# Kernel tuning notes

Measured on AMD Instinct MI355X. Metric: run time of the kernel, lower is better.

The kernel has to match this reference:

```python
import jax, jax.numpy as jnp
import numpy as np

D, DEPTH, HEADS, P, IMG = 768, 12, 12, 16, 224
GRID = IMG // P
NTOK = GRID * GRID + 1  # 197
PLEN, NTASK, NCLS = 5, 5, 100
DEEP = (2, 3, 4)
HD = D // HEADS
LN_EPS = 1e-6


def _ln(x, w, b):
    m = x.mean(-1, keepdims=True)
    v = ((x - m) ** 2).mean(-1, keepdims=True)
    return (x - m) * jax.lax.rsqrt(v + LN_EPS) * w + b


def _l2n(x):
    return x * jax.lax.rsqrt(jnp.maximum((x * x).sum(-1, keepdims=True), 1e-12))


def _mlp(x, w1, b1, w2, b2):
    return jax.nn.gelu(x @ w1.T + b1, approximate=False) @ w2.T + b2


def _mha(x, wqkv, bqkv, wp, bp):
    B, N, _ = x.shape
    qkv = (x @ wqkv.T + bqkv).reshape(B, N, 3, HEADS, HD)
    q, k, v = qkv[:, :, 0], qkv[:, :, 1], qkv[:, :, 2]
    a = jax.nn.softmax(jnp.einsum('bnhd,bmhd->bhnm', q * HD ** -0.5, k), -1)
    o = jnp.einsum('bhnm,bmhd->bnhd', a, v).reshape(B, N, D)
    return o @ wp.T + bp


def _block(x, i, p):
    x = x + _mha(_ln(x, p['ln1_w'][i], p['ln1_b'][i]), p['qkv_w'][i], p['qkv_b'][i], p['proj_w'][i], p['proj_b'][i])
    return x + _mlp(_ln(x, p['ln2_w'][i], p['ln2_b'][i]), p['fc1_w'][i], p['fc1_b'][i], p['fc2_w'][i], p['fc2_b'][i])


def _blocks(x, p):
    for i in range(DEPTH):
        x = _block(x, i, p)
    return x


def _deep_block(x, i, li, prompts, p):
    # single-head prefix-prompt attention exactly as written in the torch module,
    # including the (buggy but faithful) transpose(1,2).reshape(B,N,C) scramble
    B, N, _ = x.shape
    nx = _ln(x, p['ln1_w'][i], p['ln1_b'][i])
    qkv = (nx @ p['qkv_w'][i].T + p['qkv_b'][i]).reshape(B, N, 3, D)
    q, k, v = qkv[:, :, 0], qkv[:, :, 1], qkv[:, :, 2]
    k = jnp.concatenate([prompts[:, 2 * li], k], axis=1)
    v = jnp.concatenate([prompts[:, 2 * li + 1], v], axis=1)
    a = jax.nn.softmax(jnp.einsum('bnd,bmd->bnm', q, k) * HD ** -0.5, -1)
    av = jnp.einsum('bnm,bmd->bnd', a, v)
    av = av.swapaxes(1, 2).reshape(B, N, D)
    x = x + (av @ p['proj_w'][i].T + p['proj_b'][i])
    return x + _mlp(_ln(x, p['ln2_w'][i], p['ln2_b'][i]), p['fc1_w'][i], p['fc1_b'][i], p['fc2_w'][i], p['fc2_b'][i])


def _embed(inputs, patch_w, patch_b, cls_token, pos_embed):
    B = inputs.shape[0]
    x = inputs.reshape(B, 3, GRID, P, GRID, P).transpose(0, 2, 4, 1, 3, 5).reshape(B, GRID * GRID, 3 * P * P)
    x = x @ patch_w.T + patch_b
    x = jnp.concatenate([jnp.broadcast_to(cls_token, (B, 1, D)), x], axis=1)
    return x + pos_embed


def _branch_forward(x, sel_main, main_idx, sub_idx, p, main_prompts, sub_prompt, pos_embed, fc_w, fc_b, norm_w, norm_b):
    B = x.shape[0]
    # ---- main branch: per-sample gathered deep prompts ----
    mx = x[main_idx]
    mp = main_prompts[sel_main].reshape(mx.shape[0], 2 * len(DEEP), PLEN, D)
    for i in range(DEPTH):
        if i in DEEP:
            mx = _deep_block(mx, i, DEEP.index(i), mp, p)
        else:
            mx = _block(mx, i, p)
    mx = _ln(mx, norm_w, norm_b)
    mlog = mx[:, 0] @ fc_w.T + fc_b  # fc_norm is Identity in timm vit_base
    # ---- sub branch: prepend sub prompts after cls ----
    sx = x[sub_idx]
    sp = jnp.broadcast_to(sub_prompt[0] + pos_embed[0, 0], (sx.shape[0], PLEN, D))
    sx = jnp.concatenate([sx[:, :1], sp, sx[:, 1:]], axis=1)
    sx = _ln(_blocks(sx, p), norm_w, norm_b)
    slog = sx[:, 1:1 + PLEN].mean(axis=1) @ fc_w.T + fc_b
    # scatter back to per-sample logits (fixed output shape)
    return jnp.zeros((B, NCLS), x.dtype).at[main_idx].set(mlog).at[sub_idx].set(slog)


def setup_inputs() -> dict:
    key = jax.random.key(0)
    ks = iter(jax.random.split(key, 32))
    nk = lambda: next(ks)
    r = lambda shape, sc=0.02: jax.random.normal(nk(), shape, jnp.float32) * sc
    return {
        'inputs': jax.random.normal(nk(), (16, 3, IMG, IMG), jnp.float32),
        'task_id': 4,
        'patch_w': r((D, 3 * P * P)),
        'patch_b': jnp.zeros((D,)),
        'cls_token': r((1, 1, D)),
        'pos_embed': r((1, NTOK, D)),
        'qkv_w': r((DEPTH, 3 * D, D)),
        'qkv_b': jnp.zeros((DEPTH, 3 * D)),
        'proj_w': r((DEPTH, D, D)),
        'proj_b': jnp.zeros((DEPTH, D)),
        'ln1_w': jnp.ones((DEPTH, D)), 'ln1_b': jnp.zeros((DEPTH, D)),
        'ln2_w': jnp.ones((DEPTH, D)), 'ln2_b': jnp.zeros((DEPTH, D)),
        'fc1_w': r((DEPTH, 4 * D, D)),
        'fc1_b': jnp.zeros((DEPTH, 4 * D)),
        'fc2_w': r((DEPTH, D, 4 * D)),
        'fc2_b': jnp.zeros((DEPTH, D)),
        'norm_w': jnp.ones((D,)), 'norm_b': jnp.zeros((D,)),
        'fc_w': r((NCLS, D)),
        'fc_b': jnp.zeros((NCLS,)),
        'main_key': r((NTASK, D), 1.0),
        'sub_key': r((1, D), 1.0),
        'main_prompts': r((NTASK, 1, 2, len(DEEP), PLEN, D), 1.0),
        'sub_prompt': r((1, PLEN, D), 1.0),
    }


def reference(inputs, task_id, patch_w, patch_b, cls_token, pos_embed, qkv_w, qkv_b, proj_w, proj_b,
              ln1_w, ln1_b, ln2_w, ln2_b, fc1_w, fc1_b, fc2_w, fc2_b, norm_w, norm_b, fc_w, fc_b,
              main_key, sub_key, main_prompts, sub_prompt):
    p = dict(qkv_w=qkv_w, qkv_b=qkv_b, proj_w=proj_w, proj_b=proj_b, ln1_w=ln1_w, ln1_b=ln1_b,
             ln2_w=ln2_w, ln2_b=ln2_b, fc1_w=fc1_w, fc1_b=fc1_b, fc2_w=fc2_w, fc2_b=fc2_b)
    x = _embed(inputs, patch_w, patch_b, cls_token, pos_embed)
    # frozen query pass (torch.no_grad in the original)
    query = _ln(_blocks(x, p), norm_w, norm_b)[:, 0]
    # test-time routing: cosine similarity to [main_key[:task_id+1], sub_key]
    cand = jnp.concatenate([main_key[:task_id + 1], sub_key], axis=0)
    sim = _l2n(query) @ _l2n(cand).T
    sel = jnp.argmax(sim, axis=1)  # selection_size == 1
    main_mask = sel <= task_id
    main_idx = jnp.nonzero(main_mask)[0]
    sub_idx = jnp.nonzero(jnp.logical_not(main_mask))[0]
    sel_main = sel[main_idx]
    return _branch_forward(x, sel_main, main_idx, sub_idx, p, main_prompts, sub_prompt, pos_embed,
                           fc_w, fc_b, norm_w, norm_b)
```

## Files before the change

### kernel.cpp

```cpp
#include <hip/hip_runtime.h>
#include <math.h>

#define B_    16
#define NT_   197
#define NS_   202
#define HEADS_ 12
#define DEPTH_ 12
#define NCLS_ 100
#define MROW_ (B_ * NT_)
#define SROW_ (B_ * NS_)
#define CROW_ (MROW_ + SROW_)

typedef __attribute__((ext_vector_type(8))) short short8v;
typedef __attribute__((ext_vector_type(4))) float f32x4;

__device__ __forceinline__ short f2bf(float f){
    unsigned u = __builtin_bit_cast(unsigned, f);
    unsigned r = (u + 0x7FFFu + ((u >> 16) & 1u)) >> 16;
    return (short)r;
}
__device__ __forceinline__ unsigned pk2(float a, float b){
    return (unsigned)(unsigned short)f2bf(a) | (((unsigned)(unsigned short)f2bf(b)) << 16);
}

__device__ __forceinline__ float block_reduce_sum_f(float s, float* red, int lane, int wid){
#pragma unroll
    for (int off = 32; off; off >>= 1) s += __shfl_xor(s, off);
    if (lane == 0) red[wid] = s;
    __syncthreads();
    float S = red[0] + red[1] + red[2] + red[3];
    __syncthreads();
    return S;
}
__device__ __forceinline__ double block_reduce_sum_d(double s, double* red, int lane, int wid){
#pragma unroll
    for (int off = 32; off; off >>= 1) s += __shfl_xor(s, off);
    if (lane == 0) red[wid] = s;
    __syncthreads();
    double S = red[0] + red[1] + red[2] + red[3];
    __syncthreads();
    return S;
}

__global__ void convert_w_k(const float* __restrict__ in, short* __restrict__ out, long n){
    long i = ((long)blockIdx.x * 256 + threadIdx.x) * 8;
    long stride = (long)gridDim.x * 256 * 8;
    for (; i < n; i += stride){
        float4 a = *(const float4*)(in + i);
        float4 b = *(const float4*)(in + i + 4);
        uint4 o4;
        o4.x = pk2(a.x, a.y); o4.y = pk2(a.z, a.w);
        o4.z = pk2(b.x, b.y); o4.w = pk2(b.z, b.w);
        *(uint4*)(out + i) = o4;
    }
}

template<int EPI, int WB>
__global__ __launch_bounds__(256) void gemm_bf16(
    const short* __restrict__ A, const void* __restrict__ Wv,
    const float* __restrict__ bias, const float* __restrict__ Res,
    float* __restrict__ Cf, short* __restrict__ Cb, int M, int K, int N)
{
    __shared__ short As[128 * 48];
    __shared__ short Bs[128 * 48];
    const int t = threadIdx.x;
    const int lane = t & 63, wid = t >> 6;
    const int wr = wid >> 1, wc = wid & 1;
    const long row0 = (long)blockIdx.y * 128;
    const long col0 = (long)blockIdx.x * 128;

    f32x4 acc[4][4];
#pragma unroll
    for (int i = 0; i < 4; i++)
#pragma unroll
        for (int j = 0; j < 4; j++) acc[i][j] = (f32x4){0.f, 0.f, 0.f, 0.f};

    const int l15 = lane & 15, lkg = lane >> 4;
    const int ar = t >> 2, ac = t & 3;
    const int bn = t >> 1, bh = t & 1;

    for (int k0 = 0; k0 < K; k0 += 32){
#pragma unroll
        for (int it = 0; it < 2; it++){
            int r = ar + it * 64;
            long gr = row0 + r;
            uint4 v = {0u, 0u, 0u, 0u};
            if (gr < M) v = *(const uint4*)(A + gr * K + k0 + ac * 8);
            *(uint4*)(&As[r * 48 + ac * 8]) = v;
        }
        if (WB == 1){
            const short* Wb = (const short*)Wv;
            const short* Wp = Wb + (col0 + bn) * K + k0 + bh * 16;
            uint4 lo = *(const uint4*)(Wp);
            uint4 hi = *(const uint4*)(Wp + 8);
            *(uint4*)(&Bs[bn * 48 + bh * 16])     = lo;
            *(uint4*)(&Bs[bn * 48 + bh * 16 + 8]) = hi;
        } else {
            const float* Wf = (const float*)Wv;
            const float* Wp = Wf + (col0 + bn) * K + k0 + bh * 16;
            unsigned rr[8];
#pragma unroll
            for (int g = 0; g < 8; g++){
                float2 f = *(const float2*)(Wp + g * 2);
                rr[g] = pk2(f.x, f.y);
            }
            uint4 lo = {rr[0], rr[1], rr[2], rr[3]};
            uint4 hi = {rr[4], rr[5], rr[6], rr[7]};
            *(uint4*)(&Bs[bn * 48 + bh * 16])     = lo;
            *(uint4*)(&Bs[bn * 48 + bh * 16 + 8]) = hi;
        }
        __syncthreads();

        short8v a[4], b[4];
#pragma unroll
        for (int i = 0; i < 4; i++)
            a[i] = *(const short8v*)(&As[(wr * 64 + i * 16 + l15) * 48 + lkg * 8]);
#pragma unroll
        for (int j = 0; j < 4; j++)
            b[j] = *(const short8v*)(&Bs[(wc * 64 + j * 16 + l15) * 48 + lkg * 8]);
#pragma unroll
        for (int i = 0; i < 4; i++)
#pragma unroll
            for (int j = 0; j < 4; j++)
                acc[i][j] = __builtin_amdgcn_mfma_f32_16x16x32_bf16(a[i], b[j], acc[i][j], 0, 0, 0);
        __syncthreads();
    }

#pragma unroll
    for (int i = 0; i < 4; i++){
#pragma unroll
        for (int q = 0; q < 4; q++){
            long gr = row0 + wr * 64 + i * 16 + lkg * 4 + q;
            if (gr >= M) continue;
#pragma unroll
            for (int j = 0; j < 4; j++){
                long gc = col0 + wc * 64 + j * 16 + l15;
                float v = acc[i][j][q] + bias[gc];
                if (EPI == 1){
                    v = 0.5f * v * (1.f + erff(v * 0.70710678118654752f));
                    Cb[gr * N + gc] = f2bf(v);
                } else if (EPI == 2){
                    Cf[gr * N + gc] = v + Res[gr * N + gc];
                } else {
                    Cf[gr * N + gc] = v;
                }
            }
        }
    }
}

__global__ __launch_bounds__(256) void ln_k(const float* __restrict__ x,
    const float* __restrict__ w, const float* __restrict__ b,
    short* __restrict__ y)
{
    __shared__ float red[4];
    int row = blockIdx.x, t = threadIdx.x;
    int lane = t & 63, wid = t >> 6;
    const float* xr = x + (long)row * 768;
    float v0 = xr[t], v1 = xr[t + 256], v2 = xr[t + 512];
    float S = block_reduce_sum_f(v0 + v1 + v2, red, lane, wid);
    float m = S * (1.f / 768.f);
    float d0 = v0 - m, d1 = v1 - m, d2 = v2 - m;
    float Q = block_reduce_sum_f(d0*d0 + d1*d1 + d2*d2, red, lane, wid);
    float rs = 1.f / sqrtf(Q * (1.f / 768.f) + 1e-6f);
    short* yr = y + (long)row * 768;
    yr[t]       = f2bf(d0 * rs * w[t]       + b[t]);
    yr[t + 256] = f2bf(d1 * rs * w[t + 256] + b[t + 256]);
    yr[t + 512] = f2bf(d2 * rs * w[t + 512] + b[t + 512]);
}

__global__ __launch_bounds__(512) void attn_mfma(
    const float* __restrict__ qkv0, short* __restrict__ o0, int N0,
    const float* __restrict__ qkv1, short* __restrict__ o1, int N1)
{
    __shared__ short Ks[208 * 72];
    __shared__ short Vs[64 * 232];
    __shared__ short Ps[8 * 16 * 232];
    const int bh = blockIdx.x;
    const int b = bh / HEADS_, h = bh % HEADS_;
    const int seg = blockIdx.y;
    const float* qkv = seg ? qkv1 : qkv0;
    short* o = seg ? o1 : o0;
    const int Ntok = seg ? N1 : N0;
    const int t = threadIdx.x, lane = t & 63, wid = t >> 6;
    const long rb = (long)b * Ntok;

    {
        const int r = t >> 2, c = (t & 3) * 16;
#pragma unroll
        for (int pass = 0; pass < 2; pass++){
            int m = r + pass * 128;
            if (m < 208){
                if (m < Ntok){
                    const float* kr = qkv + (rb + m) * 2304 + 768  + h * 64 + c;
                    const float* vr = qkv + (rb + m) * 2304 + 1536 + h * 64 + c;
#pragma unroll
                    for (int j = 0; j < 16; j += 4){
                        float4 f = *(const float4*)(kr + j);
                        *(unsigned*)(&Ks[m * 72 + c + j])     = pk2(f.x, f.y);
                        *(unsigned*)(&Ks[m * 72 + c + j + 2]) = pk2(f.z, f.w);
                    }
#pragma unroll
                    for (int j = 0; j < 16; j += 4){
                        float4 f = *(const float4*)(vr + j);
                        Vs[(c + j    ) * 232 + m] = f2bf(f.x);
                        Vs[(c + j + 1) * 232 + m] = f2bf(f.y);
                        Vs[(c + j + 2) * 232 + m] = f2bf(f.z);
                        Vs[(c + j + 3) * 232 + m] = f2bf(f.w);
                    }
                } else {
#pragma unroll
                    for (int j = 0; j < 16; j += 2)
                        *(unsigned*)(&Ks[m * 72 + c + j]) = 0u;
#pragma unroll
                    for (int j = 0; j < 16; j++)
                        Vs[(c + j) * 232 + m] = 0;
                }
            }
        }
        for (int i = t; i < 64 * 16; i += 512){
            int d = i >> 4, m = 208 + (i & 15);
            Vs[d * 232 + m] = 0;
        }
        for (int i = t; i < 8 * 16 * 16; i += 512){
            int w = i >> 8, rr = (i >> 4) & 15, m = 208 + (i & 15);
            Ps[(w * 16 + rr) * 232 + m] = 0;
        }
    }
    __syncthreads();

    const int l15 = lane & 15, lkg = lane >> 4;
    short* Pw = &Ps[wid * 16 * 232];

    for (int s = wid; s < 13; s += 8){
        const int q0 = s * 16;
        short8v a0, a1;
        {
            int qrow = q0 + l15;
            if (qrow < Ntok){
                const float* qp = qkv + (rb + qrow) * 2304 + h * 64;
                float4 f0 = *(const float4*)(qp + lkg * 8);
                float4 f1 = *(const float4*)(qp + lkg * 8 + 4);
                float4 f2 = *(const float4*)(qp + 32 + lkg * 8);
                float4 f3 = *(const float4*)(qp + 32 + lkg * 8 + 4);
                unsigned u0 = pk2(f0.x * 0.125f, f0.y * 0.125f);
                unsigned u1 = pk2(f0.z * 0.125f, f0.w * 0.125f);
                unsigned u2 = pk2(f1.x * 0.125f, f1.y * 0.125f);
                unsigned u3 = pk2(f1.z * 0.125f, f1.w * 0.125f);
                unsigned v0 = pk2(f2.x * 0.125f, f2.y * 0.125f);
                unsigned v1 = pk2(f2.z * 0.125f, f2.w * 0.125f);
                unsigned v2 = pk2(f3.x * 0.125f, f3.y * 0.125f);
                unsigned v3 = pk2(f3.z * 0.125f, f3.w * 0.125f);
                uint4 ua = {u0, u1, u2, u3}, ub = {v0, v1, v2, v3};
                a0 = __builtin_bit_cast(short8v, ua);
                a1 = __builtin_bit_cast(short8v, ub);
            } else {
                uint4 z = {0u,0u,0u,0u};
                a0 = __builtin_bit_cast(short8v, z);
                a1 = __builtin_bit_cast(short8v, z);
            }
        }
        f32x4 sacc[13];
#pragma unroll
        for (int j = 0; j < 13; j++){
            short8v b0 = *(const short8v*)(&Ks[(j * 16 + l15) * 72 + lkg * 8]);
            short8v b1 = *(const short8v*)(&Ks[(j * 16 + l15) * 72 + 32 + lkg * 8]);
            f32x4 z = {0.f, 0.f, 0.f, 0.f};
            z = __builtin_amdgcn_mfma_f32_16x16x32_bf16(a0, b0, z, 0, 0, 0);
            z = __builtin_amdgcn_mfma_f32_16x16x32_bf16(a1, b1, z, 0, 0, 0);
            sacc[j] = z;
        }
#pragma unroll
        for (int j = 0; j < 13; j++){
            if (j * 16 + l15 >= Ntok){
                sacc[j][0] = -1e30f; sacc[j][1] = -1e30f;
                sacc[j][2] = -1e30f; sacc[j][3] = -1e30f;
            }
        }
#pragma unroll
        for (int rr = 0; rr < 4; rr++){
            float mx = sacc[0][rr];
#pragma unroll
            for (int j = 1; j < 13; j++) mx = fmaxf(mx, sacc[j][rr]);
            mx = fmaxf(mx, __shfl_xor(mx, 1));
            mx = fmaxf(mx, __shfl_xor(mx, 2));
            mx = fmaxf(mx, __shfl_xor(mx, 4));
            mx = fmaxf(mx, __shfl_xor(mx, 8));
            float pv[13];
            float sum = 0.f;
#pragma unroll
            for (int j = 0; j < 13; j++){
                float e = expf(sacc[j][rr] - mx);
                pv[j] = e; sum += e;
            }
            sum += __shfl_xor(sum, 1);
            sum += __shfl_xor(sum, 2);
            sum += __shfl_xor(sum, 4);
            sum += __shfl_xor(sum, 8);
            float inv = 1.f / sum;
#pragma unroll
            for (int j = 0; j < 13; j++)
                Pw[(lkg * 4 + rr) * 232 + j * 16 + l15] = f2bf(pv[j] * inv);
        }
        short8v pa[7];
#pragma unroll
        for (int kc = 0; kc < 7; kc++)
            pa[kc] = *(const short8v*)(&Pw[l15 * 232 + kc * 32 + lkg * 8]);
#pragma unroll
        for (int dj = 0; dj < 4; dj++){
            f32x4 oacc = {0.f, 0.f, 0.f, 0.f};
#pragma unroll
            for (int kc = 0; kc < 7; kc++){
                short8v vb = *(const short8v*)(&Vs[(dj * 16 + l15) * 232 + kc * 32 + lkg * 8]);
                oacc = __builtin_amdgcn_mfma_f32_16x16x32_bf16(pa[kc], vb, oacc, 0, 0, 0);
            }
#pragma unroll
            for (int rr = 0; rr < 4; rr++){
                int q = q0 + lkg * 4 + rr;
                if (q < Ntok)
                    o[(rb + q) * 768 + h * 64 + dj * 16 + l15] = f2bf(oacc[rr]);
            }
        }
    }
}

__global__ __launch_bounds__(256) void attn_deep_v2(
    const float* __restrict__ qkv, const float* __restrict__ prompts,
    const int* __restrict__ selm, short* __restrict__ o, int li)
{
    __shared__ float q[768];
    __shared__ float sc[256];
    __shared__ float red[256];
    const int b = blockIdx.x, n = blockIdx.y, t = threadIdx.x;
    const int lane = t & 63, w = t >> 6;
    const float* qr = qkv + (long)(b * NT_ + n) * 2304;
    q[t] = qr[t]; q[t + 256] = qr[t + 256]; q[t + 512] = qr[t + 512];
    __syncthreads();

    const float4 q0 = *(const float4*)(&q[lane * 4]);
    const float4 q1 = *(const float4*)(&q[256 + lane * 4]);
    const float4 q2 = *(const float4*)(&q[512 + lane * 4]);

    const float* kp = prompts + ((long)selm[b] * 6 + 2 * li) * 5 * 768;
    const float* vp = kp + 5 * 768;

    for (int m = w; m < 202; m += 4){
        const float* kr = (m < 5) ? (kp + (long)m * 768)
                                  : (qkv + (long)(b * NT_ + (m - 5)) * 2304 + 768);
        float4 k0 = *(const float4*)(kr + lane * 4);
        float4 k1 = *(const float4*)(kr + 256 + lane * 4);
        float4 k2 = *(const float4*)(kr + 512 + lane * 4);
        float a = q0.x*k0.x + q0.y*k0.y + q0.z*k0.z + q0.w*k0.w
                + q1.x*k1.x + q1.y*k1.y + q1.z*k1.z + q1.w*k1.w
                + q2.x*k2.x + q2.y*k2.y + q2.z*k2.z + q2.w*k2.w;
#pragma unroll
        for (int off = 32; off; off >>= 1) a += __shfl_xor(a, off);
        if (lane == 0) sc[m] = a * 0.125f;
    }
    __syncthreads();

    float s = (t < 202) ? sc[t] : -1e30f;
    red[t] = s; __syncthreads();
    for (int wd = 128; wd; wd >>= 1){ if (t < wd) red[t] = fmaxf(red[t], red[t+wd]); __syncthreads(); }
    float mx = red[0]; __syncthreads();
    float e = (t < 202) ? expf(s - mx) : 0.f;
    red[t] = e; __syncthreads();
    for (int wd = 128; wd; wd >>= 1){ if (t < wd) red[t] += red[t+wd]; __syncthreads(); }
    float inv = 1.f / red[0];
    __syncthreads();
    sc[t] = e * inv;
    __syncthreads();

    float a0 = 0.f, a1 = 0.f, a2 = 0.f;
    for (int m = 0; m < 5; m++){
        const float* vr = vp + (long)m * 768;
        float pm = sc[m];
        a0 += pm * vr[t]; a1 += pm * vr[t + 256]; a2 += pm * vr[t + 512];
    }
    for (int m = 5; m < 202; m++){
        const float* vr = qkv + (long)(b * NT_ + (m - 5)) * 2304 + 1536;
        float pm = sc[m];
        a0 += pm * vr[t]; a1 += pm * vr[t + 256]; a2 += pm * vr[t + 512];
    }
    short* ob = o + (long)b * NT_ * 768 + n;
    ob[(long)t * 197]         = f2bf(a0);
    ob[(long)(t + 256) * 197] = f2bf(a1);
    ob[(long)(t + 512) * 197] = f2bf(a2);
}

__global__ void unfold_k(const float* __restrict__ in, short* __restrict__ out){
    long i = (long)blockIdx.x * 256 + threadIdx.x;
    long total = (long)B_ * 196 * 768;
    if (i >= total) return;
    int f = (int)(i % 768); long rw = i / 768;
    int t = (int)(rw % 196); int b = (int)(rw / 196);
    int gy = t / 14, gx = t % 14;
    int c = f >> 8, rem = f & 255, py = rem >> 4, px = rem & 15;
    out[i] = f2bf(in[(((long)(b * 3 + c) * 224) + gy * 16 + py) * 224 + gx * 16 + px]);
}

__global__ void assemble_k(const float* __restrict__ pe, const float* __restrict__ cls,
    const float* __restrict__ pos, float* __restrict__ x0){
    long i = (long)blockIdx.x * 256 + threadIdx.x;
    long total = (long)B_ * NT_ * 768;
    if (i >= total) return;
    int d = (int)(i % 768); long rw = i / 768;
    int n = (int)(rw % NT_); int b = (int)(rw / NT_);
    float v;
    if (n == 0) v = cls[d] + pos[d];
    else        v = pe[((long)b * 196 + (n - 1)) * 768 + d] + pos[(long)n * 768 + d];
    x0[i] = v;
}

__global__ void copy_f(const float* __restrict__ a, float* __restrict__ b, long total){
    long i = (long)blockIdx.x * 256 + threadIdx.x;
    if (i < total) b[i] = a[i];
}

__global__ void build_sub_k(const float* __restrict__ x0, const float* __restrict__ subp,
    const float* __restrict__ pos, float* __restrict__ xSub){
    long i = (long)blockIdx.x * 256 + threadIdx.x;
    long total = (long)B_ * NS_ * 768;
    if (i >= total) return;
    int d = (int)(i % 768); long rw = i / 768;
    int n = (int)(rw % NS_); int b = (int)(rw / NS_);
    float v;
    if (n == 0)      v = x0[((long)b * NT_) * 768 + d];
    else if (n <= 5) v = subp[(n - 1) * 768 + d] + pos[d];
    else             v = x0[((long)b * NT_ + (n - 5)) * 768 + d];
    xSub[i] = v;
}

__global__ __launch_bounds__(256) void select_k(
    const float* __restrict__ xA, const float* __restrict__ norm_w,
    const float* __restrict__ norm_b, const float* __restrict__ main_key,
    const float* __restrict__ sub_key, const int* __restrict__ task_id_p,
    int* __restrict__ selm, int* __restrict__ flag)
{
    __shared__ double red[4];
    int b = blockIdx.x, t = threadIdx.x, lane = t & 63, wid = t >> 6;
    const float* xr = xA + (long)b * NT_ * 768;
    double v0 = xr[t], v1 = xr[t + 256], v2 = xr[t + 512];
    double S = block_reduce_sum_d(v0 + v1 + v2, red, lane, wid);
    double m = S * (1.0 / 768.0);
    double d0 = v0 - m, d1 = v1 - m, d2 = v2 - m;
    double Q = block_reduce_sum_d(d0*d0 + d1*d1 + d2*d2, red, lane, wid);
    double rs = 1.0 / sqrt(Q * (1.0 / 768.0) + 1e-6);
    double q0 = d0 * rs * (double)norm_w[t]       + (double)norm_b[t];
    double q1 = d1 * rs * (double)norm_w[t + 256] + (double)norm_b[t + 256];
    double q2 = d2 * rs * (double)norm_w[t + 512] + (double)norm_b[t + 512];
    double qn = block_reduce_sum_d(q0*q0 + q1*q1 + q2*q2, red, lane, wid);
    double qinv = 1.0 / sqrt(fmax(qn, 1e-12));

    int tk = *task_id_p;
    int ncand = tk + 2;
    double best = -1e300; int bsel = 0;
    for (int c = 0; c < ncand; c++){
        const float* cr = (c <= tk) ? (main_key + (long)c * 768) : sub_key;
        double c0 = cr[t], c1 = cr[t + 256], c2 = cr[t + 512];
        double dotq = block_reduce_sum_d(q0*c0 + q1*c1 + q2*c2, red, lane, wid);
        double nc   = block_reduce_sum_d(c0*c0 + c1*c1 + c2*c2, red, lane, wid);
        double sim = dotq * qinv * (1.0 / sqrt(fmax(nc, 1e-12)));
        if (sim > best){ best = sim; bsel = c; }
    }
    if (t == 0){
        int isMain = (bsel <= tk) ? 1 : 0;
        selm[b] = isMain ? bsel : 0;
        flag[b] = isMain;
    }
}

__global__ __launch_bounds__(256) void head_k(
    const float* __restrict__ xM, const float* __restrict__ xSub,
    const float* __restrict__ norm_w, const float* __restrict__ norm_b,
    const float* __restrict__ fc_w, const float* __restrict__ fc_b,
    const int* __restrict__ flag, float* __restrict__ out)
{
    __shared__ double vec[768];
    __shared__ double red[4];
    int b = blockIdx.x, t = threadIdx.x, lane = t & 63, wid = t >> 6;
    int isMain = flag[b];
    double a0 = 0.0, a1 = 0.0, a2 = 0.0;
    int nrows = isMain ? 1 : 5;
    for (int rI = 0; rI < nrows; rI++){
        const float* xr = isMain ? (xM + (long)b * NT_ * 768)
                                 : (xSub + ((long)b * NS_ + 1 + rI) * 768);
        double v0 = xr[t], v1 = xr[t + 256], v2 = xr[t + 512];
        double S = block_reduce_sum_d(v0 + v1 + v2, red, lane, wid);
        double m = S * (1.0 / 768.0);
        double d0 = v0 - m, d1 = v1 - m, d2 = v2 - m;
        double Q = block_reduce_sum_d(d0*d0 + d1*d1 + d2*d2, red, lane, wid);
        double rs = 1.0 / sqrt(Q * (1.0 / 768.0) + 1e-6);
        a0 += d0 * rs * (double)norm_w[t]       + (double)norm_b[t];
        a1 += d1 * rs * (double)norm_w[t + 256] + (double)norm_b[t + 256];
        a2 += d2 * rs * (double)norm_w[t + 512] + (double)norm_b[t + 512];
    }
    double scl = isMain ? 1.0 : 0.2;
    vec[t] = a0 * scl; vec[t + 256] = a1 * scl; vec[t + 512] = a2 * scl;
    __syncthreads();
    if (t < NCLS_){
        const float* wr = fc_w + (long)t * 768;
        double acc = (double)fc_b[t];
#pragma unroll 8
        for (int j = 0; j < 768; j++) acc += vec[j] * (double)wr[j];
        out[b * NCLS_ + t] = (float)acc;
    }
}

struct Params {
    const float *qkv_w, *qkv_b, *proj_w, *proj_b;
    const float *ln1_w, *ln1_b, *ln2_w, *ln2_b;
    const float *fc1_w, *fc1_b, *fc2_w, *fc2_b;
    const float *prompts; const int* selm;
    short *lnb, *attb, *hidb;
    float *qkvb;
    const short *qkv_wc, *proj_wc, *fc1_wc, *fc2_wc;
    bool cache;
};

template<int EPI>
static void launch_gemm(hipStream_t st, const short* A, const float* Wf, const short* Wc,
                        bool cache, const float* bias, const float* Res,
                        float* Cf, short* Cb, int M, int K, int N)
{
    dim3 g(N / 128, (M + 127) / 128);
    if (cache)
        gemm_bf16<EPI, 1><<<g, 256, 0, st>>>(A, (const void*)Wc, bias, Res, Cf, Cb, M, K, N);
    else
        gemm_bf16<EPI, 0><<<g, 256, 0, st>>>(A, (const void*)Wf, bias, Res, Cf, Cb, M, K, N);
}

static void run_layer(hipStream_t st, float* x, int M, int layer, int mode, int li,
                      const Params& P)
{
    ln_k<<<M, 256, 0, st>>>(x, P.ln1_w + layer * 768, P.ln1_b + layer * 768, P.lnb);
    launch_gemm<0>(st, P.lnb, P.qkv_w + (long)layer * 2304 * 768,
        P.qkv_wc + (P.cache ? (long)layer * 2304 * 768 : 0), P.cache,
        P.qkv_b + layer * 2304, nullptr, P.qkvb, nullptr, M, 768, 2304);
    if (mode == 0){
        attn_mfma<<<dim3(B_ * HEADS_, 2), 512, 0, st>>>(
            P.qkvb, P.attb, NT_,
            P.qkvb + (long)MROW_ * 2304, P.attb + (long)MROW_ * 768, NS_);
    } else if (mode == 1){
        attn_mfma<<<dim3(B_ * HEADS_, 1), 512, 0, st>>>(
            P.qkvb, P.attb, NT_, P.qkvb, P.attb, NT_);
    } else {
        attn_deep_v2<<<dim3(B_, NT_), 256, 0, st>>>(P.qkvb, P.prompts, P.selm, P.attb, li);
    }
    launch_gemm<2>(st, P.attb, P.proj_w + (long)layer * 768 * 768,
        P.proj_wc + (P.cache ? (long)layer * 768 * 768 : 0), P.cache,
        P.proj_b + layer * 768, x, x, nullptr, M, 768, 768);
    ln_k<<<M, 256, 0, st>>>(x, P.ln2_w + layer * 768, P.ln2_b + layer * 768, P.lnb);
    launch_gemm<1>(st, P.lnb, P.fc1_w + (long)layer * 3072 * 768,
        P.fc1_wc + (P.cache ? (long)layer * 3072 * 768 : 0), P.cache,
        P.fc1_b + layer * 3072, nullptr, nullptr, P.hidb, M, 768, 3072);
    launch_gemm<2>(st, P.hidb, P.fc2_w + (long)layer * 768 * 3072,
        P.fc2_wc + (P.cache ? (long)layer * 768 * 3072 : 0), P.cache,
        P.fc2_b + layer * 768, x, x, nullptr, M, 3072, 768);
}

extern "C" void kernel_launch(void* const* d_in, const int* in_sizes, int n_in,
                              void* d_out, int out_size, void* d_ws, size_t ws_size,
                              hipStream_t stream)
{
    (void)in_sizes; (void)n_in; (void)out_size;
    const float* inputs   = (const float*)d_in[0];
    const int*   task_id  = (const int*)  d_in[1];
    const float* patch_w  = (const float*)d_in[2];
    const float* patch_b  = (const float*)d_in[3];
    const float* cls_tok  = (const float*)d_in[4];
    const float* pos      = (const float*)d_in[5];
    const float* qkv_w    = (const float*)d_in[6];
    const float* qkv_b    = (const float*)d_in[7];
    const float* proj_w   = (const float*)d_in[8];
    const float* proj_b   = (const float*)d_in[9];
    const float* ln1_w    = (const float*)d_in[10];
    const float* ln1_b    = (const float*)d_in[11];
    const float* ln2_w    = (const float*)d_in[12];
    const float* ln2_b    = (const float*)d_in[13];
    const float* fc1_w    = (const float*)d_in[14];
    const float* fc1_b    = (const float*)d_in[15];
    const float* fc2_w    = (const float*)d_in[16];
    const float* fc2_b    = (const float*)d_in[17];
    const float* norm_w   = (const float*)d_in[18];
    const float* norm_b   = (const float*)d_in[19];
    const float* fc_w     = (const float*)d_in[20];
    const float* fc_b     = (const float*)d_in[21];
    const float* main_key = (const float*)d_in[22];
    const float* sub_key  = (const float*)d_in[23];
    const float* m_prompts= (const float*)d_in[24];
    const float* s_prompt = (const float*)d_in[25];
    float* out = (float*)d_out;

    char* wsb = (char*)d_ws;
    size_t off = 0;
    auto allocB = [&](size_t bytes) -> void* {
        void* p = (void*)(wsb + off);
        off += (bytes + 255) & ~(size_t)255;
        return p;
    };
    float* x0   = (float*)allocB((size_t)MROW_ * 768 * 4);
    float* xC   = (float*)allocB((size_t)CROW_ * 768 * 4);
    float* xM   = (float*)allocB((size_t)MROW_ * 768 * 4);
    short* lnb  = (short*)allocB((size_t)CROW_ * 768 * 2);
    short* attb = (short*)allocB((size_t)CROW_ * 768 * 2);
    float* qkvb = (float*)allocB((size_t)CROW_ * 2304 * 4);
    short* hidb = (short*)allocB((size_t)CROW_ * 3072 * 2);
    int*   selm = (int*)allocB(64);
    int*   flag = (int*)allocB(64);

    const size_t nQkv = (size_t)DEPTH_ * 2304 * 768;
    const size_t nProj = (size_t)DEPTH_ * 768 * 768;
    const size_t nFc1 = (size_t)DEPTH_ * 3072 * 768;
    const size_t nFc2 = (size_t)DEPTH_ * 768 * 3072;
    const size_t nPatch = (size_t)768 * 768;
    size_t cacheBytes = (nQkv + nProj + nFc1 + nFc2 + nPatch) * 2 + 5 * 256;
    bool cache = (ws_size >= off + cacheBytes + (1u << 20));
    short *qkv_wc = nullptr, *proj_wc = nullptr, *fc1_wc = nullptr, *fc2_wc = nullptr, *patch_wc = nullptr;
    if (cache){
        qkv_wc  = (short*)allocB(nQkv * 2);
        proj_wc = (short*)allocB(nProj * 2);
        fc1_wc  = (short*)allocB(nFc1 * 2);
        fc2_wc  = (short*)allocB(nFc2 * 2);
        patch_wc= (short*)allocB(nPatch * 2);
        convert_w_k<<<2048, 256, 0, stream>>>(qkv_w,  qkv_wc,  (long)nQkv);
        convert_w_k<<<1024, 256, 0, stream>>>(proj_w, proj_wc, (long)nProj);
        convert_w_k<<<2048, 256, 0, stream>>>(fc1_w,  fc1_wc,  (long)nFc1);
        convert_w_k<<<2048, 256, 0, stream>>>(fc2_w,  fc2_wc,  (long)nFc2);
        convert_w_k<<<256,  256, 0, stream>>>(patch_w, patch_wc, (long)nPatch);
    }

    Params P;
    P.qkv_w = qkv_w; P.qkv_b = qkv_b; P.proj_w = proj_w; P.proj_b = proj_b;
    P.ln1_w = ln1_w; P.ln1_b = ln1_b; P.ln2_w = ln2_w; P.ln2_b = ln2_b;
    P.fc1_w = fc1_w; P.fc1_b = fc1_b; P.fc2_w = fc2_w; P.fc2_b = fc2_b;
    P.prompts = m_prompts; P.selm = selm;
    P.lnb = lnb; P.attb = attb; P.hidb = hidb; P.qkvb = qkvb;
    P.qkv_wc = qkv_wc; P.proj_wc = proj_wc; P.fc1_wc = fc1_wc; P.fc2_wc = fc2_wc;
    P.cache = cache;

    const long XN = (long)MROW_ * 768;

    {
        long tot = (long)B_ * 196 * 768;
        short* un  = hidb;
        float* peo = qkvb;
        unfold_k<<<(int)((tot + 255) / 256), 256, 0, stream>>>(inputs, un);
        launch_gemm<0>(stream, un, patch_w, patch_wc, cache, patch_b, nullptr,
                       peo, nullptr, 3136, 768, 768);
        assemble_k<<<(int)((XN + 255) / 256), 256, 0, stream>>>(peo, cls_tok, pos, x0);
        copy_f<<<(int)((XN + 255) / 256), 256, 0, stream>>>(x0, xC, XN);
        long st = (long)SROW_ * 768;
        build_sub_k<<<(int)((st + 255) / 256), 256, 0, stream>>>(x0, s_prompt, pos,
                                                                 xC + (long)MROW_ * 768);
    }

    for (int i = 0; i < DEPTH_; i++){
        run_layer(stream, xC, CROW_, i, 0, 0, P);
        if (i == 1)
            copy_f<<<(int)((XN + 255) / 256), 256, 0, stream>>>(xC, xM, XN);
    }

    select_k<<<16, 256, 0, stream>>>(xC, norm_w, norm_b, main_key, sub_key,
                                     task_id, selm, flag);

    for (int i = 2; i < DEPTH_; i++){
        int mode = (i >= 2 && i <= 4) ? 2 : 1;
        run_layer(stream, xM, MROW_, i, mode, i - 2, P);
    }

    head_k<<<16, 256, 0, stream>>>(xM, xC + (long)MROW_ * 768, norm_w, norm_b,
                                   fc_w, fc_b, flag, out);
}
```

Measured before the change: 6.476 ms.

## Store QKV activations in bf16 and use one wave per row LayerNorm

The QKV GEMM now writes bf16 output through a new epilogue, and both attention kernels read bf16 Q/K/V directly. The 1/8 scale moves from Q onto the fp32 scores. This halves QKV write and read traffic and removes the conversion work in attention, at the cost of rounding Q before scaling. LayerNorm is reworked to process one row per wavefront with shuffle-only reductions, which drops the shared-memory block reductions and syncs. A separate buffer is allocated for the patch-embed output because the QKV buffer is now too small to hold it.

```diff
diff --git a/kernel.cpp b/kernel.cpp
--- a/kernel.cpp
+++ b/kernel.cpp
@@ -22,16 +22,20 @@
 __device__ __forceinline__ unsigned pk2(float a, float b){
     return (unsigned)(unsigned short)f2bf(a) | (((unsigned)(unsigned short)f2bf(b)) << 16);
 }
-
-__device__ __forceinline__ float block_reduce_sum_f(float s, float* red, int lane, int wid){
-#pragma unroll
-    for (int off = 32; off; off >>= 1) s += __shfl_xor(s, off);
-    if (lane == 0) red[wid] = s;
-    __syncthreads();
-    float S = red[0] + red[1] + red[2] + red[3];
-    __syncthreads();
-    return S;
-}
+__device__ __forceinline__ float bf2f(unsigned short s){
+    unsigned u = ((unsigned)s) << 16;
+    return __builtin_bit_cast(float, u);
+}
+__device__ __forceinline__ float4 ld4bf(const short* p){
+    uint2 u = *(const uint2*)p;
+    float4 r;
+    r.x = bf2f((unsigned short)(u.x & 0xffff));
+    r.y = bf2f((unsigned short)(u.x >> 16));
+    r.z = bf2f((unsigned short)(u.y & 0xffff));
+    r.w = bf2f((unsigned short)(u.y >> 16));
+    return r;
+}
+
 __device__ __forceinline__ double block_reduce_sum_d(double s, double* red, int lane, int wid){
 #pragma unroll
     for (int off = 32; off; off >>= 1) s += __shfl_xor(s, off);
@@ -141,6 +145,8 @@
                     Cb[gr * N + gc] = f2bf(v);
                 } else if (EPI == 2){
                     Cf[gr * N + gc] = v + Res[gr * N + gc];
+                } else if (EPI == 3){
+                    Cb[gr * N + gc] = f2bf(v);
                 } else {
                     Cf[gr * N + gc] = v;
                 }
@@ -151,27 +157,34 @@
 
 __global__ __launch_bounds__(256) void ln_k(const float* __restrict__ x,
     const float* __restrict__ w, const float* __restrict__ b,
-    short* __restrict__ y)
-{
-    __shared__ float red[4];
-    int row = blockIdx.x, t = threadIdx.x;
-    int lane = t & 63, wid = t >> 6;
+    short* __restrict__ y, int M)
+{
+    const int lane = threadIdx.x & 63, wv = threadIdx.x >> 6;
+    const int row = blockIdx.x * 4 + wv;
+    if (row >= M) return;
     const float* xr = x + (long)row * 768;
-    float v0 = xr[t], v1 = xr[t + 256], v2 = xr[t + 512];
-    float S = block_reduce_sum_f(v0 + v1 + v2, red, lane, wid);
-    float m = S * (1.f / 768.f);
-    float d0 = v0 - m, d1 = v1 - m, d2 = v2 - m;
-    float Q = block_reduce_sum_f(d0*d0 + d1*d1 + d2*d2, red, lane, wid);
-    float rs = 1.f / sqrtf(Q * (1.f / 768.f) + 1e-6f);
+    float v[12];
+    float s = 0.f;
+#pragma unroll
+    for (int j = 0; j < 12; j++){ v[j] = xr[lane + j * 64]; s += v[j]; }
+#pragma unroll
+    for (int off = 32; off; off >>= 1) s += __shfl_xor(s, off);
+    float m = s * (1.f / 768.f);
+    float q = 0.f;
+#pragma unroll
+    for (int j = 0; j < 12; j++){ v[j] -= m; q += v[j] * v[j]; }
+#pragma unroll
+    for (int off = 32; off; off >>= 1) q += __shfl_xor(q, off);
+    float rs = 1.f / sqrtf(q * (1.f / 768.f) + 1e-6f);
     short* yr = y + (long)row * 768;
-    yr[t]       = f2bf(d0 * rs * w[t]       + b[t]);
-    yr[t + 256] = f2bf(d1 * rs * w[t + 256] + b[t + 256]);
-    yr[t + 512] = f2bf(d2 * rs * w[t + 512] + b[t + 512]);
+#pragma unroll
+    for (int j = 0; j < 12; j++)
+        yr[lane + j * 64] = f2bf(v[j] * rs * w[lane + j * 64] + b[lane + j * 64]);
 }
 
 __global__ __launch_bounds__(512) void attn_mfma(
-    const float* __restrict__ qkv0, short* __restrict__ o0, int N0,
-    const float* __restrict__ qkv1, short* __restrict__ o1, int N1)
+    const short* __restrict__ qkv0, short* __restrict__ o0, int N0,
+    const short* __restrict__ qkv1, short* __restrict__ o1, int N1)
 {
     __shared__ short Ks[208 * 72];
     __shared__ short Vs[64 * 232];
@@ -179,7 +192,7 @@
     const int bh = blockIdx.x;
     const int b = bh / HEADS_, h = bh % HEADS_;
     const int seg = blockIdx.y;
-    const float* qkv = seg ? qkv1 : qkv0;
+    const short* qkv = seg ? qkv1 : qkv0;
     short* o = seg ? o1 : o0;
     const int Ntok = seg ? N1 : N0;
     const int t = threadIdx.x, lane = t & 63, wid = t >> 6;
@@ -192,22 +205,13 @@
             int m = r + pass * 128;
             if (m < 208){
                 if (m < Ntok){
-                    const float* kr = qkv + (rb + m) * 2304 + 768  + h * 64 + c;
-                    const float* vr = qkv + (rb + m) * 2304 + 1536 + h * 64 + c;
-#pragma unroll
-                    for (int j = 0; j < 16; j += 4){
-                        float4 f = *(const float4*)(kr + j);
-                        *(unsigned*)(&Ks[m * 72 + c + j])     = pk2(f.x, f.y);
-                        *(unsigned*)(&Ks[m * 72 + c + j + 2]) = pk2(f.z, f.w);
-                    }
-#pragma unroll
-                    for (int j = 0; j < 16; j += 4){
-                        float4 f = *(const float4*)(vr + j);
-                        Vs[(c + j    ) * 232 + m] = f2bf(f.x);
-                        Vs[(c + j + 1) * 232 + m] = f2bf(f.y);
-                        Vs[(c + j + 2) * 232 + m] = f2bf(f.z);
-                        Vs[(c + j + 3) * 232 + m] = f2bf(f.w);
-                    }
+                    const short* kr = qkv + (rb + m) * 2304 + 768  + h * 64 + c;
+                    const short* vr = qkv + (rb + m) * 2304 + 1536 + h * 64 + c;
+                    *(uint4*)(&Ks[m * 72 + c])     = *(const uint4*)(kr);
+                    *(uint4*)(&Ks[m * 72 + c + 8]) = *(const uint4*)(kr + 8);
+#pragma unroll
+                    for (int j = 0; j < 16; j++)
+                        Vs[(c + j) * 232 + m] = vr[j];
                 } else {
 #pragma unroll
                     for (int j = 0; j < 16; j += 2)
@@ -238,22 +242,9 @@
         {
             int qrow = q0 + l15;
             if (qrow < Ntok){
-                const float* qp = qkv + (rb + qrow) * 2304 + h * 64;
-                float4 f0 = *(const float4*)(qp + lkg * 8);
-                float4 f1 = *(const float4*)(qp + lkg * 8 + 4);
-                float4 f2 = *(const float4*)(qp + 32 + lkg * 8);
-                float4 f3 = *(const float4*)(qp + 32 + lkg * 8 + 4);
-                unsigned u0 = pk2(f0.x * 0.125f, f0.y * 0.125f);
-                unsigned u1 = pk2(f0.z * 0.125f, f0.w * 0.125f);
-                unsigned u2 = pk2(f1.x * 0.125f, f1.y * 0.125f);
-                unsigned u3 = pk2(f1.z * 0.125f, f1.w * 0.125f);
-                unsigned v0 = pk2(f2.x * 0.125f, f2.y * 0.125f);
-                unsigned v1 = pk2(f2.z * 0.125f, f2.w * 0.125f);
-                unsigned v2 = pk2(f3.x * 0.125f, f3.y * 0.125f);
-                unsigned v3 = pk2(f3.z * 0.125f, f3.w * 0.125f);
-                uint4 ua = {u0, u1, u2, u3}, ub = {v0, v1, v2, v3};
-                a0 = __builtin_bit_cast(short8v, ua);
-                a1 = __builtin_bit_cast(short8v, ub);
+                const short* qp = qkv + (rb + qrow) * 2304 + h * 64;
+                a0 = *(const short8v*)(qp + lkg * 8);
+                a1 = *(const short8v*)(qp + 32 + lkg * 8);
             } else {
                 uint4 z = {0u,0u,0u,0u};
                 a0 = __builtin_bit_cast(short8v, z);
@@ -268,7 +259,8 @@
             f32x4 z = {0.f, 0.f, 0.f, 0.f};
             z = __builtin_amdgcn_mfma_f32_16x16x32_bf16(a0, b0, z, 0, 0, 0);
             z = __builtin_amdgcn_mfma_f32_16x16x32_bf16(a1, b1, z, 0, 0, 0);
-            sacc[j] = z;
+            sacc[j][0] = z[0] * 0.125f; sacc[j][1] = z[1] * 0.125f;
+            sacc[j][2] = z[2] * 0.125f; sacc[j][3] = z[3] * 0.125f;
         }
 #pragma unroll
         for (int j = 0; j < 13; j++){
@@ -325,7 +317,7 @@
 }
 
 __global__ __launch_bounds__(256) void attn_deep_v2(
-    const float* __restrict__ qkv, const float* __restrict__ prompts,
+    const short* __restrict__ qkv, const float* __restrict__ prompts,
     const int* __restrict__ selm, short* __restrict__ o, int li)
 {
     __shared__ float q[768];
@@ -333,8 +325,10 @@
     __shared__ float red[256];
     const int b = blockIdx.x, n = blockIdx.y, t = threadIdx.x;
     const int lane = t & 63, w = t >> 6;
-    const float* qr = qkv + (long)(b * NT_ + n) * 2304;
-    q[t] = qr[t]; q[t + 256] = qr[t + 256]; q[t + 512] = qr[t + 512];
+    const short* qr = qkv + (long)(b * NT_ + n) * 2304;
+    q[t] = bf2f((unsigned short)qr[t]);
+    q[t + 256] = bf2f((unsigned short)qr[t + 256]);
+    q[t + 512] = bf2f((unsigned short)qr[t + 512]);
     __syncthreads();
 
     const float4 q0 = *(const float4*)(&q[lane * 4]);
@@ -345,11 +339,18 @@
     const float* vp = kp + 5 * 768;
 
     for (int m = w; m < 202; m += 4){
-        const float* kr = (m < 5) ? (kp + (long)m * 768)
-                                  : (qkv + (long)(b * NT_ + (m - 5)) * 2304 + 768);
-        float4 k0 = *(const float4*)(kr + lane * 4);
-        float4 k1 = *(const float4*)(kr + 256 + lane * 4);
-        float4 k2 = *(const float4*)(kr + 512 + lane * 4);
+        float4 k0, k1, k2;
+        if (m < 5){
+            const float* kr = kp + (long)m * 768;
+            k0 = *(const float4*)(kr + lane * 4);
+            k1 = *(const float4*)(kr + 256 + lane * 4);
+            k2 = *(const float4*)(kr + 512 + lane * 4);
+        } else {
+            const short* kr = qkv + (long)(b * NT_ + (m - 5)) * 2304 + 768;
+            k0 = ld4bf(kr + lane * 4);
+            k1 = ld4bf(kr + 256 + lane * 4);
+            k2 = ld4bf(kr + 512 + lane * 4);
+        }
         float a = q0.x*k0.x + q0.y*k0.y + q0.z*k0.z + q0.w*k0.w
                 + q1.x*k1.x + q1.y*k1.y + q1.z*k1.z + q1.w*k1.w
                 + q2.x*k2.x + q2.y*k2.y + q2.z*k2.z + q2.w*k2.w;
@@ -378,9 +379,11 @@
         a0 += pm * vr[t]; a1 += pm * vr[t + 256]; a2 += pm * vr[t + 512];
     }
     for (int m = 5; m < 202; m++){
-        const float* vr = qkv + (long)(b * NT_ + (m - 5)) * 2304 + 1536;
+        const short* vr = qkv + (long)(b * NT_ + (m - 5)) * 2304 + 1536;
         float pm = sc[m];
-        a0 += pm * vr[t]; a1 += pm * vr[t + 256]; a2 += pm * vr[t + 512];
+        a0 += pm * bf2f((unsigned short)vr[t]);
+        a1 += pm * bf2f((unsigned short)vr[t + 256]);
+        a2 += pm * bf2f((unsigned short)vr[t + 512]);
     }
     short* ob = o + (long)b * NT_ * 768 + n;
     ob[(long)t * 197]         = f2bf(a0);
@@ -513,7 +516,7 @@
     const float *fc1_w, *fc1_b, *fc2_w, *fc2_b;
     const float *prompts; const int* selm;
     short *lnb, *attb, *hidb;
-    float *qkvb;
+    short *qkvb;
     const short *qkv_wc, *proj_wc, *fc1_wc, *fc2_wc;
     bool cache;
 };
@@ -533,10 +536,11 @@
 static void run_layer(hipStream_t st, float* x, int M, int layer, int mode, int li,
                       const Params& P)
 {
-    ln_k<<<M, 256, 0, st>>>(x, P.ln1_w + layer * 768, P.ln1_b + layer * 768, P.lnb);
-    launch_gemm<0>(st, P.lnb, P.qkv_w + (long)layer * 2304 * 768,
+    int lnGrid = (M + 3) / 4;
+    ln_k<<<lnGrid, 256, 0, st>>>(x, P.ln1_w + layer * 768, P.ln1_b + layer * 768, P.lnb, M);
+    launch_gemm<3>(st, P.lnb, P.qkv_w + (long)layer * 2304 * 768,
         P.qkv_wc + (P.cache ? (long)layer * 2304 * 768 : 0), P.cache,
-        P.qkv_b + layer * 2304, nullptr, P.qkvb, nullptr, M, 768, 2304);
+        P.qkv_b + layer * 2304, nullptr, nullptr, P.qkvb, M, 768, 2304);
     if (mode == 0){
         attn_mfma<<<dim3(B_ * HEADS_, 2), 512, 0, st>>>(
             P.qkvb, P.attb, NT_,
@@ -550,7 +554,7 @@
     launch_gemm<2>(st, P.attb, P.proj_w + (long)layer * 768 * 768,
         P.proj_wc + (P.cache ? (long)layer * 768 * 768 : 0), P.cache,
         P.proj_b + layer * 768, x, x, nullptr, M, 768, 768);
-    ln_k<<<M, 256, 0, st>>>(x, P.ln2_w + layer * 768, P.ln2_b + layer * 768, P.lnb);
+    ln_k<<<lnGrid, 256, 0, st>>>(x, P.ln2_w + layer * 768, P.ln2_b + layer * 768, P.lnb, M);
     launch_gemm<1>(st, P.lnb, P.fc1_w + (long)layer * 3072 * 768,
         P.fc1_wc + (P.cache ? (long)layer * 3072 * 768 : 0), P.cache,
         P.fc1_b + layer * 3072, nullptr, nullptr, P.hidb, M, 768, 3072);
@@ -604,8 +608,9 @@
     float* xM   = (float*)allocB((size_t)MROW_ * 768 * 4);
     short* lnb  = (short*)allocB((size_t)CROW_ * 768 * 2);
     short* attb = (short*)allocB((size_t)CROW_ * 768 * 2);
-    float* qkvb = (float*)allocB((size_t)CROW_ * 2304 * 4);
+    short* qkvb = (short*)allocB((size_t)CROW_ * 2304 * 2);
     short* hidb = (short*)allocB((size_t)CROW_ * 3072 * 2);
+    float* peo  = (float*)allocB((size_t)3136 * 768 * 4);
     int*   selm = (int*)allocB(64);
     int*   flag = (int*)allocB(64);
 
@@ -643,8 +648,7 @@
 
     {
         long tot = (long)B_ * 196 * 768;
-        short* un  = hidb;
-        float* peo = qkvb;
+        short* un = hidb;
         unfold_k<<<(int)((tot + 255) / 256), 256, 0, stream>>>(inputs, un);
         launch_gemm<0>(stream, un, patch_w, patch_wc, cache, patch_b, nullptr,
                        peo, nullptr, 3136, 768, 768);
```

Measured after the change: 6.336 ms. 2.2% less time.
